# Optimization experiments

Measured on AMD Instinct MI355X. Metric: run time of the kernel, lower is better.

Reference implementation:

```python
import jax, jax.numpy as jnp
import numpy as np

NEG_INF = -1.0e10


def setup_inputs() -> dict:
    key = jax.random.key(0)
    ks = jax.random.split(key, 6)
    B, T, S = 64, 128, 512
    ENC, DEC = 1024, 512
    dec_hidden = jax.random.normal(ks[0], (B, T, DEC), dtype=jnp.float32)
    encoder_hiddens = jax.random.normal(ks[1], (B, S, ENC), dtype=jnp.float32)
    encoder_mask = jax.random.randint(ks[2], (B, S), 0, 2, dtype=jnp.int32)
    # nn.Linear(enc_dim, dec_dim) weight stored as [ENC, DEC] (already transposed)
    W_attn = jax.random.normal(ks[3], (ENC, DEC), dtype=jnp.float32) * (ENC ** -0.5)
    b_attn = jax.random.normal(ks[4], (DEC,), dtype=jnp.float32) * 0.01
    # linear_out: nn.Linear(enc_dim + dec_dim, dec_dim, bias=False)
    W_out = jax.random.normal(ks[5], (ENC + DEC, DEC), dtype=jnp.float32) * ((ENC + DEC) ** -0.5)
    return {
        "dec_hidden": dec_hidden,
        "encoder_hiddens": encoder_hiddens,
        "encoder_mask": encoder_mask,
        "W_attn": W_attn,
        "b_attn": b_attn,
        "W_out": W_out,
    }


def reference(dec_hidden, encoder_hiddens, encoder_mask, W_attn, b_attn, W_out):
    # --- score (method='general') ---
    maskf = encoder_mask.astype(dec_hidden.dtype)  # [B, S]
    proj = jnp.einsum("bse,ed->bsd", encoder_hiddens, W_attn) + b_attn  # [B, S, D]
    proj = proj * maskf[:, :, None]
    energies = jnp.einsum("btd,bsd->bts", dec_hidden, proj)  # [B, T, S]
    # --- mask-add + softmax ---
    neg_mask = NEG_INF * (1.0 - maskf)[:, None, :]  # [B, 1, S]
    masked_energies = energies + neg_mask
    attn_weights = jax.nn.softmax(masked_energies, axis=-1)  # [B, T, S]
    # --- weighted context + concat + linear_out + tanh ---
    weighted_context = jnp.einsum("bts,bse->bte", attn_weights, encoder_hiddens)
    h_cat = jnp.concatenate([weighted_context, dec_hidden], axis=-1)  # [B, T, E+D]
    h_tilde = jnp.tanh(jnp.einsum("btc,cd->btd", h_cat, W_out))  # [B, T, D]
    return h_tilde, attn_weights, masked_energies
```

## Files before the change

kernel.cpp:

```cpp
#include <hip/hip_runtime.h>
#include <cmath>

#define BB 64
#define TT 128
#define SS 512
#define EE 1024
#define DDIM 512
#define NEG_INF_F (-1.0e10f)

#define BM 128
#define BN 64
#define BK 32
#define LDSTP 20
#define ROWU 32

typedef unsigned short u16;
typedef __attribute__((ext_vector_type(8))) short bf16x8;
typedef __attribute__((ext_vector_type(4))) float f32x4;

__device__ __forceinline__ unsigned bf16_rne(float f) {
    unsigned u = __float_as_uint(f);
    return (u + 0x7fffu + ((u >> 16) & 1u)) >> 16;
}
__device__ __forceinline__ void split2(float f, unsigned& h, unsigned& l) {
    h = bf16_rne(f);
    float fh = __uint_as_float(h << 16);
    l = bf16_rne(f - fh);
}

template <int ROWS>
__device__ __forceinline__ void stage_glds(u16* lds, const u16* __restrict__ src,
                                           int ld, int tid) {
    const int w = tid >> 6, lane = tid & 63;
    const int rl = lane >> 2, p = lane & 3;
#pragma unroll
    for (int i = 0; i < ROWS / 64; ++i) {
        const int r0 = (w + 4 * i) * 16;
        const int r = r0 + rl;
        const int q = p ^ ((r >> 1) & 3);
        const u16* g = src + (size_t)r * ld + 8 * q;
        __builtin_amdgcn_global_load_lds(
            (const __attribute__((address_space(1))) unsigned*)g,
            (__attribute__((address_space(3))) unsigned*)(lds + r0 * ROWU),
            16, 0, 0);
    }
}

__device__ __forceinline__ bf16x8 read_frag_sw(const u16* buf, int row, int q) {
    const int c = q ^ ((row >> 1) & 3);
    return *(const bf16x8*)(buf + row * ROWU + 8 * c);
}

template <int ROWS>
__device__ __forceinline__ void stage_nt(unsigned* hi, unsigned* lo,
                                         const float* __restrict__ src, int ld, int tid) {
#pragma unroll
    for (int i = 0; i < ROWS / 32; ++i) {
        int s = tid + 256 * i;
        int r = s >> 3, kq = s & 7;
        float4 v = *(const float4*)(src + (size_t)r * ld + 4 * kq);
        unsigned h0, l0, h1, l1, h2, l2, h3, l3;
        split2(v.x, h0, l0); split2(v.y, h1, l1);
        split2(v.z, h2, l2); split2(v.w, h3, l3);
        *(uint2*)&hi[r * LDSTP + 2 * kq] = make_uint2(h0 | (h1 << 16), h2 | (h3 << 16));
        *(uint2*)&lo[r * LDSTP + 2 * kq] = make_uint2(l0 | (l1 << 16), l2 | (l3 << 16));
    }
}

__device__ __forceinline__ void stage_tr(unsigned* hi, unsigned* lo,
                                         const float* __restrict__ src, int ld, int tid) {
    int eq = tid & 15;
    int sp = tid >> 4;
    const float* p = src + (size_t)(2 * sp) * ld + 4 * eq;
    float4 va = *(const float4*)p;
    float4 vb = *(const float4*)(p + ld);
    float av[4] = {va.x, va.y, va.z, va.w};
    float bv[4] = {vb.x, vb.y, vb.z, vb.w};
#pragma unroll
    for (int c = 0; c < 4; ++c) {
        unsigned ha, la, hb, lb;
        split2(av[c], ha, la);
        split2(bv[c], hb, lb);
        hi[(4 * eq + c) * LDSTP + sp] = ha | (hb << 16);
        lo[(4 * eq + c) * LDSTP + sp] = la | (lb << 16);
    }
}

__device__ __forceinline__ bf16x8 read_frag_pad(const unsigned* buf, int row, int q) {
    return *(const bf16x8*)(buf + row * LDSTP + 4 * q);
}

__device__ __forceinline__ void mfma_ss(const u16* Ah, const u16* Al,
                                        const u16* Bh, const u16* Bl,
                                        f32x4 acc[4][2], int tid) {
    const int lane = tid & 63, w = tid >> 6;
    const int wm = (w & 1) * 64, wn = (w >> 1) * 32;
    const int fr = lane & 15, q = lane >> 4;
    bf16x8 ah[4], al[4];
#pragma unroll
    for (int i = 0; i < 4; ++i) {
        ah[i] = read_frag_sw(Ah, wm + 16 * i + fr, q);
        al[i] = read_frag_sw(Al, wm + 16 * i + fr, q);
    }
#pragma unroll
    for (int j = 0; j < 2; ++j) {
        bf16x8 bh = read_frag_sw(Bh, wn + 16 * j + fr, q);
        bf16x8 bl = read_frag_sw(Bl, wn + 16 * j + fr, q);
#pragma unroll
        for (int i = 0; i < 4; ++i) {
            acc[i][j] = __builtin_amdgcn_mfma_f32_16x16x32_bf16(ah[i], bh, acc[i][j], 0, 0, 0);
            acc[i][j] = __builtin_amdgcn_mfma_f32_16x16x32_bf16(ah[i], bl, acc[i][j], 0, 0, 0);
            acc[i][j] = __builtin_amdgcn_mfma_f32_16x16x32_bf16(al[i], bh, acc[i][j], 0, 0, 0);
        }
    }
}

__device__ __forceinline__ void mfma_sp(const u16* Ah, const u16* Al,
                                        const unsigned* Bh, const unsigned* Bl,
                                        f32x4 acc[4][2], int tid) {
    const int lane = tid & 63, w = tid >> 6;
    const int wm = (w & 1) * 64, wn = (w >> 1) * 32;
    const int fr = lane & 15, q = lane >> 4;
    bf16x8 ah[4], al[4];
#pragma unroll
    for (int i = 0; i < 4; ++i) {
        ah[i] = read_frag_sw(Ah, wm + 16 * i + fr, q);
        al[i] = read_frag_sw(Al, wm + 16 * i + fr, q);
    }
#pragma unroll
    for (int j = 0; j < 2; ++j) {
        bf16x8 bh = read_frag_pad(Bh, wn + 16 * j + fr, q);
        bf16x8 bl = read_frag_pad(Bl, wn + 16 * j + fr, q);
#pragma unroll
        for (int i = 0; i < 4; ++i) {
            acc[i][j] = __builtin_amdgcn_mfma_f32_16x16x32_bf16(ah[i], bh, acc[i][j], 0, 0, 0);
            acc[i][j] = __builtin_amdgcn_mfma_f32_16x16x32_bf16(ah[i], bl, acc[i][j], 0, 0, 0);
            acc[i][j] = __builtin_amdgcn_mfma_f32_16x16x32_bf16(al[i], bh, acc[i][j], 0, 0, 0);
        }
    }
}

__global__ __launch_bounds__(256) void k_conv(const float* __restrict__ src,
                                              u16* __restrict__ hi, u16* __restrict__ lo) {
    const int i = blockIdx.x * 256 + threadIdx.x;
    float4 v = ((const float4*)src)[i];
    unsigned h0, l0, h1, l1, h2, l2, h3, l3;
    split2(v.x, h0, l0); split2(v.y, h1, l1);
    split2(v.z, h2, l2); split2(v.w, h3, l3);
    ((ushort4*)hi)[i] = make_ushort4((u16)h0, (u16)h1, (u16)h2, (u16)h3);
    ((ushort4*)lo)[i] = make_ushort4((u16)l0, (u16)l1, (u16)l2, (u16)l3);
}

__global__ __launch_bounds__(256) void k_wot(const float* __restrict__ Wo,
                                             u16* __restrict__ thi, u16* __restrict__ tlo) {
    __shared__ float t[64][65];
    const int tid = threadIdx.x;
    const int r0 = blockIdx.x * 64;
    const int c0 = blockIdx.y * 64;
    const int rr = tid >> 4, cc = tid & 15;
#pragma unroll
    for (int i = 0; i < 4; ++i) {
        float4 v = *(const float4*)(Wo + (size_t)(r0 + rr + 16 * i) * DDIM + c0 + 4 * cc);
        t[rr + 16 * i][4 * cc + 0] = v.x;
        t[rr + 16 * i][4 * cc + 1] = v.y;
        t[rr + 16 * i][4 * cc + 2] = v.z;
        t[rr + 16 * i][4 * cc + 3] = v.w;
    }
    __syncthreads();
#pragma unroll
    for (int i = 0; i < 4; ++i) {
        const int oc = rr + 16 * i;
        unsigned h0, l0, h1, l1, h2, l2, h3, l3;
        split2(t[4 * cc + 0][oc], h0, l0);
        split2(t[4 * cc + 1][oc], h1, l1);
        split2(t[4 * cc + 2][oc], h2, l2);
        split2(t[4 * cc + 3][oc], h3, l3);
        size_t off = (size_t)(c0 + oc) * (EE + DDIM) + r0 + 4 * cc;
        *(ushort4*)(thi + off) = make_ushort4((u16)h0, (u16)h1, (u16)h2, (u16)h3);
        *(ushort4*)(tlo + off) = make_ushort4((u16)l0, (u16)l1, (u16)l2, (u16)l3);
    }
}

__global__ __launch_bounds__(256) void k_decw(const u16* __restrict__ Ahp, const u16* __restrict__ Alp,
                                              const u16* __restrict__ Bhp, const u16* __restrict__ Blp,
                                              u16* __restrict__ Chi, u16* __restrict__ Clo) {
    __shared__ u16 Ah[BM * ROWU], Al[BM * ROWU], Bh[BN * ROWU], Bl[BN * ROWU];
    const int tid = threadIdx.x;
    const int bm = blockIdx.x * BM, bn = blockIdx.y * BN;
    f32x4 acc[4][2] = {};
    for (int k0 = 0; k0 < DDIM; k0 += BK) {
        __syncthreads();
        stage_glds<BM>(Ah, Ahp + (size_t)bm * DDIM + k0, DDIM, tid);
        stage_glds<BM>(Al, Alp + (size_t)bm * DDIM + k0, DDIM, tid);
        stage_glds<BN>(Bh, Bhp + (size_t)bn * DDIM + k0, DDIM, tid);
        stage_glds<BN>(Bl, Blp + (size_t)bn * DDIM + k0, DDIM, tid);
        __builtin_amdgcn_s_waitcnt(0);
        __syncthreads();
        mfma_ss(Ah, Al, Bh, Bl, acc, tid);
    }
    const int lane = tid & 63, w = tid >> 6;
    const int wm = (w & 1) * 64, wn = (w >> 1) * 32;
    const int fr = lane & 15, q = lane >> 4;
#pragma unroll
    for (int j = 0; j < 2; ++j) {
        const int col = bn + wn + 16 * j + fr;
#pragma unroll
        for (int i = 0; i < 4; ++i)
#pragma unroll
            for (int r = 0; r < 4; ++r) {
                const int row = bm + wm + 16 * i + 4 * q + r;
                unsigned h, l;
                split2(acc[i][j][r], h, l);
                Chi[(size_t)row * EE + col] = (u16)h;
                Clo[(size_t)row * EE + col] = (u16)l;
            }
    }
}

__global__ __launch_bounds__(256) void k_decb(const float* __restrict__ dec,
                                              const float* __restrict__ ba,
                                              float* __restrict__ decb) {
    const int row = blockIdx.x * 4 + (threadIdx.x >> 6);
    const int lane = threadIdx.x & 63;
    const float* x = dec + (size_t)row * DDIM;
    float s = 0.f;
#pragma unroll
    for (int i = 0; i < 8; ++i) {
        int idx = lane + i * 64;
        s += x[idx] * ba[idx];
    }
#pragma unroll
    for (int off = 32; off >= 1; off >>= 1) s += __shfl_xor(s, off, 64);
    if (lane == 0) decb[row] = s;
}

__global__ __launch_bounds__(256) void k_energy(const u16* __restrict__ Ahp, const u16* __restrict__ Alp,
                                                const float* __restrict__ enc,
                                                const int* __restrict__ mask,
                                                const float* __restrict__ decb,
                                                float* __restrict__ menerg) {
    const int b = blockIdx.z;
    const int bn = blockIdx.x * BN;
    __shared__ u16 Ah[BM * ROWU], Al[BM * ROWU];
    __shared__ unsigned Bh[BN * LDSTP], Bl[BN * LDSTP];
    const int tid = threadIdx.x;
    const u16* Abh = Ahp + (size_t)b * TT * EE;
    const u16* Abl = Alp + (size_t)b * TT * EE;
    const float* Bt = enc + (size_t)b * SS * EE + (size_t)bn * EE;
    f32x4 acc[4][2] = {};
    for (int k0 = 0; k0 < EE; k0 += BK) {
        __syncthreads();
        stage_glds<BM>(Ah, Abh + k0, EE, tid);
        stage_glds<BM>(Al, Abl + k0, EE, tid);
        stage_nt<BN>(Bh, Bl, Bt + k0, EE, tid);
        __builtin_amdgcn_s_waitcnt(0);
        __syncthreads();
        mfma_sp(Ah, Al, Bh, Bl, acc, tid);
    }
    const int lane = tid & 63, w = tid >> 6;
    const int wm = (w & 1) * 64, wn = (w >> 1) * 32;
    const int fr = lane & 15, q = lane >> 4;
    const int* mb = mask + (size_t)b * SS;
    const float* dbp = decb + (size_t)b * TT;
    float* Crow = menerg + (size_t)b * TT * SS;
    float db[4][4];
#pragma unroll
    for (int i = 0; i < 4; ++i) {
        float4 d4 = *(const float4*)(dbp + wm + 16 * i + 4 * q);
        db[i][0] = d4.x; db[i][1] = d4.y; db[i][2] = d4.z; db[i][3] = d4.w;
    }
#pragma unroll
    for (int j = 0; j < 2; ++j) {
        const int col = bn + wn + 16 * j + fr;
        const int mk = mb[col];
#pragma unroll
        for (int i = 0; i < 4; ++i)
#pragma unroll
            for (int r = 0; r < 4; ++r) {
                const int row = wm + 16 * i + 4 * q + r;
                Crow[(size_t)row * SS + col] = mk ? acc[i][j][r] + db[i][r] : NEG_INF_F;
            }
    }
}

__global__ __launch_bounds__(128) void k_softmax(const float* __restrict__ me,
                                                 float* __restrict__ attn,
                                                 u16* __restrict__ ahi,
                                                 u16* __restrict__ alo) {
    const int row = blockIdx.x;
    const int tid = threadIdx.x;
    const float4 v = ((const float4*)(me + (size_t)row * SS))[tid];
    float m = fmaxf(fmaxf(v.x, v.y), fmaxf(v.z, v.w));
#pragma unroll
    for (int off = 32; off >= 1; off >>= 1) m = fmaxf(m, __shfl_xor(m, off, 64));
    __shared__ float redm[2];
    __shared__ float reds[2];
    const int wv = tid >> 6, lane = tid & 63;
    if (lane == 0) redm[wv] = m;
    __syncthreads();
    m = fmaxf(redm[0], redm[1]);
    float e0 = __expf(v.x - m), e1 = __expf(v.y - m);
    float e2 = __expf(v.z - m), e3 = __expf(v.w - m);
    float s = (e0 + e1) + (e2 + e3);
#pragma unroll
    for (int off = 32; off >= 1; off >>= 1) s += __shfl_xor(s, off, 64);
    if (lane == 0) reds[wv] = s;
    __syncthreads();
    s = reds[0] + reds[1];
    const float inv = 1.0f / s;
    float o0 = e0 * inv, o1 = e1 * inv, o2 = e2 * inv, o3 = e3 * inv;
    ((float4*)(attn + (size_t)row * SS))[tid] = make_float4(o0, o1, o2, o3);
    unsigned h0, l0, h1, l1, h2, l2, h3, l3;
    split2(o0, h0, l0); split2(o1, h1, l1); split2(o2, h2, l2); split2(o3, h3, l3);
    ((ushort4*)(ahi + (size_t)row * SS))[tid] = make_ushort4((u16)h0, (u16)h1, (u16)h2, (u16)h3);
    ((ushort4*)(alo + (size_t)row * SS))[tid] = make_ushort4((u16)l0, (u16)l1, (u16)l2, (u16)l3);
}

__global__ __launch_bounds__(256) void k_ctx(const u16* __restrict__ Ahp, const u16* __restrict__ Alp,
                                             const float* __restrict__ enc,
                                             u16* __restrict__ Chi, u16* __restrict__ Clo) {
    const int b = blockIdx.z;
    const int bn = blockIdx.x * BN;
    __shared__ u16 Ah[BM * ROWU], Al[BM * ROWU];
    __shared__ unsigned Bh[BN * LDSTP], Bl[BN * LDSTP];
    const int tid = threadIdx.x;
    const u16* Abh = Ahp + (size_t)b * TT * SS;
    const u16* Abl = Alp + (size_t)b * TT * SS;
    const float* Bm = enc + (size_t)b * SS * EE + bn;
    f32x4 acc[4][2] = {};
    for (int k0 = 0; k0 < SS; k0 += BK) {
        __syncthreads();
        stage_glds<BM>(Ah, Abh + k0, SS, tid);
        stage_glds<BM>(Al, Abl + k0, SS, tid);
        stage_tr(Bh, Bl, Bm + (size_t)k0 * EE, EE, tid);
        __builtin_amdgcn_s_waitcnt(0);
        __syncthreads();
        mfma_sp(Ah, Al, Bh, Bl, acc, tid);
    }
    const int lane = tid & 63, w = tid >> 6;
    const int wm = (w & 1) * 64, wn = (w >> 1) * 32;
    const int fr = lane & 15, q = lane >> 4;
    u16* Ch = Chi + (size_t)b * TT * EE;
    u16* Cl = Clo + (size_t)b * TT * EE;
#pragma unroll
    for (int j = 0; j < 2; ++j) {
        const int col = bn + wn + 16 * j + fr;
#pragma unroll
        for (int i = 0; i < 4; ++i)
#pragma unroll
            for (int r = 0; r < 4; ++r) {
                const int row = wm + 16 * i + 4 * q + r;
                unsigned h, l;
                split2(acc[i][j][r], h, l);
                Ch[(size_t)row * EE + col] = (u16)h;
                Cl[(size_t)row * EE + col] = (u16)l;
            }
    }
}

__global__ __launch_bounds__(256) void k_out(const u16* __restrict__ wch, const u16* __restrict__ wcl,
                                             const u16* __restrict__ dech, const u16* __restrict__ decl,
                                             const u16* __restrict__ woth, const u16* __restrict__ wotl,
                                             float* __restrict__ ht) {
    __shared__ u16 Ah[BM * ROWU], Al[BM * ROWU], Bh[BN * ROWU], Bl[BN * ROWU];
    const int tid = threadIdx.x;
    const int bm = blockIdx.x * BM, bn = blockIdx.y * BN;
    f32x4 acc[4][2] = {};
    for (int k0 = 0; k0 < EE + DDIM; k0 += BK) {
        const u16 *ah, *al;
        int ld;
        if (k0 < EE) {
            ah = wch + (size_t)bm * EE + k0;
            al = wcl + (size_t)bm * EE + k0;
            ld = EE;
        } else {
            ah = dech + (size_t)bm * DDIM + (k0 - EE);
            al = decl + (size_t)bm * DDIM + (k0 - EE);
            ld = DDIM;
        }
        __syncthreads();
        stage_glds<BM>(Ah, ah, ld, tid);
        stage_glds<BM>(Al, al, ld, tid);
        stage_glds<BN>(Bh, woth + (size_t)bn * (EE + DDIM) + k0, EE + DDIM, tid);
        stage_glds<BN>(Bl, wotl + (size_t)bn * (EE + DDIM) + k0, EE + DDIM, tid);
        __builtin_amdgcn_s_waitcnt(0);
        __syncthreads();
        mfma_ss(Ah, Al, Bh, Bl, acc, tid);
    }
    const int lane = tid & 63, w = tid >> 6;
    const int wm = (w & 1) * 64, wn = (w >> 1) * 32;
    const int fr = lane & 15, q = lane >> 4;
#pragma unroll
    for (int j = 0; j < 2; ++j) {
        const int col = bn + wn + 16 * j + fr;
#pragma unroll
        for (int i = 0; i < 4; ++i)
#pragma unroll
            for (int r = 0; r < 4; ++r) {
                const int row = bm + wm + 16 * i + 4 * q + r;
                ht[(size_t)row * DDIM + col] = tanhf(acc[i][j][r]);
            }
    }
}

extern "C" void kernel_launch(void* const* d_in, const int* in_sizes, int n_in,
                              void* d_out, int out_size, void* d_ws, size_t ws_size,
                              hipStream_t stream) {
    (void)in_sizes; (void)n_in; (void)out_size; (void)ws_size;
    const float* dec = (const float*)d_in[0];
    const float* enc = (const float*)d_in[1];
    const int* mask = (const int*)d_in[2];
    const float* Wa = (const float*)d_in[3];
    const float* ba = (const float*)d_in[4];
    const float* Wo = (const float*)d_in[5];

    float* h_tilde = (float*)d_out;
    float* attn = h_tilde + (size_t)BB * TT * DDIM;
    float* menerg = attn + (size_t)BB * TT * SS;

    char* ws = (char*)d_ws;
    u16* decW_hi = (u16*)(ws);
    u16* decW_lo = (u16*)(ws + 16777216);
    u16* dec_hi  = (u16*)(ws + 33554432);
    u16* dec_lo  = (u16*)(ws + 41943040);
    u16* attn_hi = (u16*)(ws + 50331648);
    u16* attn_lo = (u16*)(ws + 58720256);
    u16* wa_hi   = (u16*)(ws + 67108864);
    u16* wa_lo   = (u16*)(ws + 68157440);
    u16* wot_hi  = (u16*)(ws + 69206016);
    u16* wot_lo  = (u16*)(ws + 70778880);
    float* decb  = (float*)(ws + 72351744);
    u16* wc_hi = decW_hi;
    u16* wc_lo = decW_lo;

    k_conv<<<(BB * TT * DDIM) / 4 / 256, 256, 0, stream>>>(dec, dec_hi, dec_lo);
    k_conv<<<(EE * DDIM) / 4 / 256, 256, 0, stream>>>(Wa, wa_hi, wa_lo);
    k_wot<<<dim3((EE + DDIM) / 64, DDIM / 64), 256, 0, stream>>>(Wo, wot_hi, wot_lo);
    k_decb<<<(BB * TT) / 4, 256, 0, stream>>>(dec, ba, decb);
    k_decw<<<dim3((BB * TT) / BM, EE / BN), 256, 0, stream>>>(dec_hi, dec_lo, wa_hi, wa_lo,
                                                              decW_hi, decW_lo);
    k_energy<<<dim3(SS / BN, 1, BB), 256, 0, stream>>>(decW_hi, decW_lo, enc, mask, decb, menerg);
    k_softmax<<<BB * TT, 128, 0, stream>>>(menerg, attn, attn_hi, attn_lo);
    k_ctx<<<dim3(EE / BN, 1, BB), 256, 0, stream>>>(attn_hi, attn_lo, enc, wc_hi, wc_lo);
    k_out<<<dim3((BB * TT) / BM, DDIM / BN), 256, 0, stream>>>(wc_hi, wc_lo, dec_hi, dec_lo,
                                                               wot_hi, wot_lo, h_tilde);
}
```

Baseline: 409.2 us.

## Double-buffer LDS tiles to overlap global loads with MFMA in all GEMM kernels

Converts the four GEMM kernels (decw, energy, context, out) from single-buffered LDS staging to a two-stage ping-pong pipeline. The next K-tile is fetched with global_load_lds (and register-held fp32 loads for the split hi/lo B operand) while MFMAs run on the current buffer, with one barrier per iteration instead of two. The aim is to hide global memory latency behind compute. In exchange LDS use per block doubles, which may lower occupancy, and the register-staged loads raise register pressure.

```diff
diff --git a/kernel.cpp b/kernel.cpp
--- a/kernel.cpp
+++ b/kernel.cpp
@@ -51,31 +51,43 @@
     return *(const bf16x8*)(buf + row * ROWU + 8 * c);
 }
 
-template <int ROWS>
-__device__ __forceinline__ void stage_nt(unsigned* hi, unsigned* lo,
-                                         const float* __restrict__ src, int ld, int tid) {
-#pragma unroll
-    for (int i = 0; i < ROWS / 32; ++i) {
+__device__ __forceinline__ void stage_nt_load(float4* v, const float* __restrict__ src,
+                                              int ld, int tid) {
+#pragma unroll
+    for (int i = 0; i < 2; ++i) {
         int s = tid + 256 * i;
         int r = s >> 3, kq = s & 7;
-        float4 v = *(const float4*)(src + (size_t)r * ld + 4 * kq);
+        v[i] = *(const float4*)(src + (size_t)r * ld + 4 * kq);
+    }
+}
+__device__ __forceinline__ void stage_nt_store(unsigned* hi, unsigned* lo,
+                                               const float4* v, int tid) {
+#pragma unroll
+    for (int i = 0; i < 2; ++i) {
+        int s = tid + 256 * i;
+        int r = s >> 3, kq = s & 7;
         unsigned h0, l0, h1, l1, h2, l2, h3, l3;
-        split2(v.x, h0, l0); split2(v.y, h1, l1);
-        split2(v.z, h2, l2); split2(v.w, h3, l3);
+        split2(v[i].x, h0, l0); split2(v[i].y, h1, l1);
+        split2(v[i].z, h2, l2); split2(v[i].w, h3, l3);
         *(uint2*)&hi[r * LDSTP + 2 * kq] = make_uint2(h0 | (h1 << 16), h2 | (h3 << 16));
         *(uint2*)&lo[r * LDSTP + 2 * kq] = make_uint2(l0 | (l1 << 16), l2 | (l3 << 16));
     }
 }
 
-__device__ __forceinline__ void stage_tr(unsigned* hi, unsigned* lo,
-                                         const float* __restrict__ src, int ld, int tid) {
+__device__ __forceinline__ void stage_tr_load(float4* v, const float* __restrict__ src,
+                                              int ld, int tid) {
     int eq = tid & 15;
     int sp = tid >> 4;
     const float* p = src + (size_t)(2 * sp) * ld + 4 * eq;
-    float4 va = *(const float4*)p;
-    float4 vb = *(const float4*)(p + ld);
-    float av[4] = {va.x, va.y, va.z, va.w};
-    float bv[4] = {vb.x, vb.y, vb.z, vb.w};
+    v[0] = *(const float4*)p;
+    v[1] = *(const float4*)(p + ld);
+}
+__device__ __forceinline__ void stage_tr_store(unsigned* hi, unsigned* lo,
+                                               const float4* v, int tid) {
+    int eq = tid & 15;
+    int sp = tid >> 4;
+    float av[4] = {v[0].x, v[0].y, v[0].z, v[0].w};
+    float bv[4] = {v[1].x, v[1].y, v[1].z, v[1].w};
 #pragma unroll
     for (int c = 0; c < 4; ++c) {
         unsigned ha, la, hb, lb;
@@ -184,20 +196,32 @@
 __global__ __launch_bounds__(256) void k_decw(const u16* __restrict__ Ahp, const u16* __restrict__ Alp,
                                               const u16* __restrict__ Bhp, const u16* __restrict__ Blp,
                                               u16* __restrict__ Chi, u16* __restrict__ Clo) {
-    __shared__ u16 Ah[BM * ROWU], Al[BM * ROWU], Bh[BN * ROWU], Bl[BN * ROWU];
+    __shared__ u16 Ah[2][BM * ROWU], Al[2][BM * ROWU], Bh[2][BN * ROWU], Bl[2][BN * ROWU];
     const int tid = threadIdx.x;
     const int bm = blockIdx.x * BM, bn = blockIdx.y * BN;
+    const u16* Ahs = Ahp + (size_t)bm * DDIM;
+    const u16* Als = Alp + (size_t)bm * DDIM;
+    const u16* Bhs = Bhp + (size_t)bn * DDIM;
+    const u16* Bls = Blp + (size_t)bn * DDIM;
     f32x4 acc[4][2] = {};
-    for (int k0 = 0; k0 < DDIM; k0 += BK) {
-        __syncthreads();
-        stage_glds<BM>(Ah, Ahp + (size_t)bm * DDIM + k0, DDIM, tid);
-        stage_glds<BM>(Al, Alp + (size_t)bm * DDIM + k0, DDIM, tid);
-        stage_glds<BN>(Bh, Bhp + (size_t)bn * DDIM + k0, DDIM, tid);
-        stage_glds<BN>(Bl, Blp + (size_t)bn * DDIM + k0, DDIM, tid);
+    stage_glds<BM>(Ah[0], Ahs, DDIM, tid);
+    stage_glds<BM>(Al[0], Als, DDIM, tid);
+    stage_glds<BN>(Bh[0], Bhs, DDIM, tid);
+    stage_glds<BN>(Bl[0], Bls, DDIM, tid);
+    __builtin_amdgcn_s_waitcnt(0);
+    __syncthreads();
+    int cur = 0;
+    for (int k0 = BK; k0 < DDIM; k0 += BK) {
+        stage_glds<BM>(Ah[cur ^ 1], Ahs + k0, DDIM, tid);
+        stage_glds<BM>(Al[cur ^ 1], Als + k0, DDIM, tid);
+        stage_glds<BN>(Bh[cur ^ 1], Bhs + k0, DDIM, tid);
+        stage_glds<BN>(Bl[cur ^ 1], Bls + k0, DDIM, tid);
+        mfma_ss(Ah[cur], Al[cur], Bh[cur], Bl[cur], acc, tid);
         __builtin_amdgcn_s_waitcnt(0);
         __syncthreads();
-        mfma_ss(Ah, Al, Bh, Bl, acc, tid);
-    }
+        cur ^= 1;
+    }
+    mfma_ss(Ah[cur], Al[cur], Bh[cur], Bl[cur], acc, tid);
     const int lane = tid & 63, w = tid >> 6;
     const int wm = (w & 1) * 64, wn = (w >> 1) * 32;
     const int fr = lane & 15, q = lane >> 4;
@@ -241,22 +265,32 @@
                                                 float* __restrict__ menerg) {
     const int b = blockIdx.z;
     const int bn = blockIdx.x * BN;
-    __shared__ u16 Ah[BM * ROWU], Al[BM * ROWU];
-    __shared__ unsigned Bh[BN * LDSTP], Bl[BN * LDSTP];
+    __shared__ u16 Ah[2][BM * ROWU], Al[2][BM * ROWU];
+    __shared__ unsigned Bh[2][BN * LDSTP], Bl[2][BN * LDSTP];
     const int tid = threadIdx.x;
     const u16* Abh = Ahp + (size_t)b * TT * EE;
     const u16* Abl = Alp + (size_t)b * TT * EE;
     const float* Bt = enc + (size_t)b * SS * EE + (size_t)bn * EE;
     f32x4 acc[4][2] = {};
-    for (int k0 = 0; k0 < EE; k0 += BK) {
-        __syncthreads();
-        stage_glds<BM>(Ah, Abh + k0, EE, tid);
-        stage_glds<BM>(Al, Abl + k0, EE, tid);
-        stage_nt<BN>(Bh, Bl, Bt + k0, EE, tid);
+    float4 bv[2];
+    stage_glds<BM>(Ah[0], Abh, EE, tid);
+    stage_glds<BM>(Al[0], Abl, EE, tid);
+    stage_nt_load(bv, Bt, EE, tid);
+    stage_nt_store(Bh[0], Bl[0], bv, tid);
+    __builtin_amdgcn_s_waitcnt(0);
+    __syncthreads();
+    int cur = 0;
+    for (int k0 = BK; k0 < EE; k0 += BK) {
+        stage_nt_load(bv, Bt + k0, EE, tid);
+        stage_glds<BM>(Ah[cur ^ 1], Abh + k0, EE, tid);
+        stage_glds<BM>(Al[cur ^ 1], Abl + k0, EE, tid);
+        mfma_sp(Ah[cur], Al[cur], Bh[cur], Bl[cur], acc, tid);
+        stage_nt_store(Bh[cur ^ 1], Bl[cur ^ 1], bv, tid);
         __builtin_amdgcn_s_waitcnt(0);
         __syncthreads();
-        mfma_sp(Ah, Al, Bh, Bl, acc, tid);
-    }
+        cur ^= 1;
+    }
+    mfma_sp(Ah[cur], Al[cur], Bh[cur], Bl[cur], acc, tid);
     const int lane = tid & 63, w = tid >> 6;
     const int wm = (w & 1) * 64, wn = (w >> 1) * 32;
     const int fr = lane & 15, q = lane >> 4;
@@ -321,22 +355,32 @@
                                              u16* __restrict__ Chi, u16* __restrict__ Clo) {
     const int b = blockIdx.z;
     const int bn = blockIdx.x * BN;
-    __shared__ u16 Ah[BM * ROWU], Al[BM * ROWU];
-    __shared__ unsigned Bh[BN * LDSTP], Bl[BN * LDSTP];
+    __shared__ u16 Ah[2][BM * ROWU], Al[2][BM * ROWU];
+    __shared__ unsigned Bh[2][BN * LDSTP], Bl[2][BN * LDSTP];
     const int tid = threadIdx.x;
     const u16* Abh = Ahp + (size_t)b * TT * SS;
     const u16* Abl = Alp + (size_t)b * TT * SS;
     const float* Bm = enc + (size_t)b * SS * EE + bn;
     f32x4 acc[4][2] = {};
-    for (int k0 = 0; k0 < SS; k0 += BK) {
-        __syncthreads();
-        stage_glds<BM>(Ah, Abh + k0, SS, tid);
-        stage_glds<BM>(Al, Abl + k0, SS, tid);
-        stage_tr(Bh, Bl, Bm + (size_t)k0 * EE, EE, tid);
+    float4 bv[2];
+    stage_glds<BM>(Ah[0], Abh, SS, tid);
+    stage_glds<BM>(Al[0], Abl, SS, tid);
+    stage_tr_load(bv, Bm, EE, tid);
+    stage_tr_store(Bh[0], Bl[0], bv, tid);
+    __builtin_amdgcn_s_waitcnt(0);
+    __syncthreads();
+    int cur = 0;
+    for (int k0 = BK; k0 < SS; k0 += BK) {
+        stage_tr_load(bv, Bm + (size_t)k0 * EE, EE, tid);
+        stage_glds<BM>(Ah[cur ^ 1], Abh + k0, SS, tid);
+        stage_glds<BM>(Al[cur ^ 1], Abl + k0, SS, tid);
+        mfma_sp(Ah[cur], Al[cur], Bh[cur], Bl[cur], acc, tid);
+        stage_tr_store(Bh[cur ^ 1], Bl[cur ^ 1], bv, tid);
         __builtin_amdgcn_s_waitcnt(0);
         __syncthreads();
-        mfma_sp(Ah, Al, Bh, Bl, acc, tid);
-    }
+        cur ^= 1;
+    }
+    mfma_sp(Ah[cur], Al[cur], Bh[cur], Bl[cur], acc, tid);
     const int lane = tid & 63, w = tid >> 6;
     const int wm = (w & 1) * 64, wn = (w >> 1) * 32;
     const int fr = lane & 15, q = lane >> 4;
@@ -362,11 +406,19 @@
                                              const u16* __restrict__ dech, const u16* __restrict__ decl,
                                              const u16* __restrict__ woth, const u16* __restrict__ wotl,
                                              float* __restrict__ ht) {
-    __shared__ u16 Ah[BM * ROWU], Al[BM * ROWU], Bh[BN * ROWU], Bl[BN * ROWU];
+    __shared__ u16 Ah[2][BM * ROWU], Al[2][BM * ROWU], Bh[2][BN * ROWU], Bl[2][BN * ROWU];
     const int tid = threadIdx.x;
     const int bm = blockIdx.x * BM, bn = blockIdx.y * BN;
+    const int KTOT = EE + DDIM;
     f32x4 acc[4][2] = {};
-    for (int k0 = 0; k0 < EE + DDIM; k0 += BK) {
+    stage_glds<BM>(Ah[0], wch + (size_t)bm * EE, EE, tid);
+    stage_glds<BM>(Al[0], wcl + (size_t)bm * EE, EE, tid);
+    stage_glds<BN>(Bh[0], woth + (size_t)bn * KTOT, KTOT, tid);
+    stage_glds<BN>(Bl[0], wotl + (size_t)bn * KTOT, KTOT, tid);
+    __builtin_amdgcn_s_waitcnt(0);
+    __syncthreads();
+    int cur = 0;
+    for (int k0 = BK; k0 < KTOT; k0 += BK) {
         const u16 *ah, *al;
         int ld;
         if (k0 < EE) {
@@ -378,15 +430,16 @@
             al = decl + (size_t)bm * DDIM + (k0 - EE);
             ld = DDIM;
         }
-        __syncthreads();
-        stage_glds<BM>(Ah, ah, ld, tid);
-        stage_glds<BM>(Al, al, ld, tid);
-        stage_glds<BN>(Bh, woth + (size_t)bn * (EE + DDIM) + k0, EE + DDIM, tid);
-        stage_glds<BN>(Bl, wotl + (size_t)bn * (EE + DDIM) + k0, EE + DDIM, tid);
+        stage_glds<BM>(Ah[cur ^ 1], ah, ld, tid);
+        stage_glds<BM>(Al[cur ^ 1], al, ld, tid);
+        stage_glds<BN>(Bh[cur ^ 1], woth + (size_t)bn * KTOT + k0, KTOT, tid);
+        stage_glds<BN>(Bl[cur ^ 1], wotl + (size_t)bn * KTOT + k0, KTOT, tid);
+        mfma_ss(Ah[cur], Al[cur], Bh[cur], Bl[cur], acc, tid);
         __builtin_amdgcn_s_waitcnt(0);
         __syncthreads();
-        mfma_ss(Ah, Al, Bh, Bl, acc, tid);
-    }
+        cur ^= 1;
+    }
+    mfma_ss(Ah[cur], Al[cur], Bh[cur], Bl[cur], acc, tid);
     const int lane = tid & 63, w = tid >> 6;
     const int wm = (w & 1) * 64, wn = (w >> 1) * 32;
     const int fr = lane & 15, q = lane >> 4;
```

After: 450.6 us. 1.1x slower.
